# Kernel optimization log

Measured on AMD Instinct MI355X. Metric: run time of the kernel, lower is better.

Reference implementation:

```python
import jax, jax.numpy as jnp
import numpy as np

B, N, H, MEM, V = 512, 50, 256, 8, 40001
SCALE = 1.0 / float(np.sqrt(H))
NEG = -1e12


def sinusoid_table(n_pos, d):
    pos = np.arange(n_pos)[:, None].astype(np.float64)
    j = np.arange(d)[None, :]
    ang = pos / np.power(10000.0, 2 * (j // 2) / d)
    tab = np.zeros((n_pos, d))
    tab[:, 0::2] = np.sin(ang[:, 0::2])
    tab[:, 1::2] = np.cos(ang[:, 1::2])
    return jnp.asarray(tab, jnp.float32)

TAB = sinusoid_table(N, H)


def setup_inputs():
    key = jax.random.key(0)
    ks = jax.random.split(key, 40)
    s = 0.05
    rn = lambda k, shp, sc=s: jax.random.normal(k, shp, jnp.float32) * sc
    lengths = jax.random.randint(ks[0], (B,), 1, N + 1)
    mask = (jnp.arange(N)[None, :] < lengths[:, None]).astype(jnp.int32)
    item_flag = jax.random.randint(ks[1], (B, V - 1), 0, 2).astype(jnp.int32)
    inp = {
        'seq_emb_1': rn(ks[2], (B, N, H), 1.0),
        'seq_emb_2': rn(ks[3], (B, N, H), 1.0),
        'mask': mask,
        'item_flag': item_flag,
        # 2-layer GRU (torch layout: W_ih [3H,H], W_hh [3H,H])
        'gru_wih0': rn(ks[4], (3 * H, H)), 'gru_whh0': rn(ks[5], (3 * H, H)),
        'gru_bih0': rn(ks[6], (3 * H,)), 'gru_bhh0': rn(ks[7], (3 * H,)),
        'gru_wih1': rn(ks[8], (3 * H, H)), 'gru_whh1': rn(ks[9], (3 * H, H)),
        'gru_bih1': rn(ks[10], (3 * H,)), 'gru_bhh1': rn(ks[11], (3 * H,)),
        # attention projections ([in,out] layout, y = x @ W)
        'Wq1': rn(ks[12], (H, H)), 'Wk1': rn(ks[13], (H, H)), 'Wv1': rn(ks[14], (H, H)),
        'Wq2': rn(ks[15], (H, H)), 'Wk2': rn(ks[16], (H, H)), 'Wv2': rn(ks[17], (H, H)),
        'W_ffn1': rn(ks[18], (H, H)), 'b_ffn1': rn(ks[19], (H,)),
        'W_ffn2': rn(ks[20], (H, H)), 'b_ffn2': rn(ks[21], (H,)),
        'W_one1': rn(ks[22], (H, H)), 'b_one1': rn(ks[23], (H,)),
        'W_three1': rn(ks[24], (2 * H, 1)),
        'W_trans1': rn(ks[25], (2 * H, H)), 'b_trans1': rn(ks[26], (H,)),
        'W_tail1': rn(ks[27], (H, H)), 'b_tail1': rn(ks[28], (H,)),
        'W_tail2': rn(ks[29], (H, 2)),
        'mem_k': rn(ks[30], (1, MEM, H)), 'mem_v': rn(ks[31], (1, MEM, H)),
        'emb1': rn(ks[32], (V, H)),
    }
    return inp


def _gru_layer(x, wih, whh, bih, bhh):
    # x: [B,N,H] -> [B,N,H], h0 = 0 (torch default)
    def step(h, xt):
        gi = xt @ wih.T + bih
        gh = h @ whh.T + bhh
        ir, iz, inn = jnp.split(gi, 3, axis=-1)
        hr, hz, hn = jnp.split(gh, 3, axis=-1)
        r = jax.nn.sigmoid(ir + hr)
        z = jax.nn.sigmoid(iz + hz)
        n = jnp.tanh(inn + r * hn)
        h2 = (1.0 - z) * n + z * h
        return h2, h2
    h0 = jnp.zeros((x.shape[0], H), x.dtype)
    _, ys = jax.lax.scan(step, h0, jnp.swapaxes(x, 0, 1))
    return jnp.swapaxes(ys, 0, 1)


def _co_attention(q, k, v, mask, mem_k=None, mem_v=None):
    b = q.shape[0]
    causal = jnp.tril(jnp.ones((N, N), bool))           # [N,N]
    pad = mask.astype(bool)[:, None, :]                  # [B,1,N]
    allow_seq = causal[None, :, :] & pad                 # [B,N,N]
    if mem_k is not None:
        k = jnp.concatenate([jnp.broadcast_to(mem_k, (b, MEM, H)), k], axis=1)
        v = jnp.concatenate([jnp.broadcast_to(mem_v, (b, MEM, H)), v], axis=1)
        mem_ok = jnp.ones((b, N, MEM), bool)             # memory keys always visible
        allow = jnp.concatenate([mem_ok, allow_seq], axis=-1)
    else:
        allow = allow_seq
    att = jnp.einsum('bqh,bkh->bqk', q, k) * SCALE
    att = jax.nn.softmax(jnp.where(allow, att, NEG), axis=-1)
    return jnp.einsum('bqk,bkh->bqh', att, v) * mask[:, :, None].astype(q.dtype)


def reference(seq_emb_1, seq_emb_2, mask, item_flag,
              gru_wih0, gru_whh0, gru_bih0, gru_bhh0,
              gru_wih1, gru_whh1, gru_bih1, gru_bhh1,
              Wq1, Wk1, Wv1, Wq2, Wk2, Wv2,
              W_ffn1, b_ffn1, W_ffn2, b_ffn2,
              W_one1, b_one1, W_three1, W_trans1, b_trans1,
              W_tail1, b_tail1, W_tail2, mem_k, mem_v, emb1):
    b = mask.shape[0]
    mf = mask[:, :, None].astype(jnp.float32)
    # 2-layer GRU on stream 2
    s2 = _gru_layer(seq_emb_2, gru_wih0, gru_whh0, gru_bih0, gru_bhh0)
    s2 = _gru_layer(s2, gru_wih1, gru_whh1, gru_bih1, gru_bhh1)
    last = jnp.sum(mask, axis=1) - 1                     # last valid index
    sr_l_1 = seq_emb_1[jnp.arange(b), last]              # [B,H]
    q1_1 = sr_l_1 @ W_one1 + b_one1 + TAB[0]
    se1 = seq_emb_1 * mf
    # positional encoding indexed by |pos - last_idx|
    flag = jnp.abs(jnp.arange(N, dtype=jnp.int32)[None, :] - last[:, None].astype(jnp.int32))
    pe = TAB[flag]                                       # [B,N,H]
    q1 = se1 @ Wq1 + pe
    k1 = se1 @ Wk1 + pe
    v1 = se1 @ Wv1 + pe
    att1 = _co_attention(q1, k1, v1, mask) @ W_ffn1 + b_ffn1
    se2 = s2 * mf
    k2 = se2 @ Wk2
    v2 = se2 @ Wv2
    att2 = _co_attention(q1, k2, v2, mask, mem_k, mem_v) @ W_ffn2 + b_ffn2
    att = jax.nn.relu(att1 + att2)
    alpha = jnp.concatenate([att, jnp.broadcast_to(q1_1[:, None, :], att.shape)], axis=-1) @ W_three1
    alpha = jax.nn.softmax(jnp.where(mf > 0, alpha, NEG), axis=1)  # [B,N,1]
    sess = jnp.sum(alpha * se1 * mf, axis=1)
    sess = jnp.concatenate([sess, sr_l_1], axis=1) @ W_trans1 + b_trans1
    item_emb = emb1[1:]                                  # [V-1,H]
    score = sess @ item_emb.T                            # [B,V-1]
    fl = item_flag.astype(bool)
    score_in = jax.nn.softmax(jnp.where(fl, score, NEG), axis=-1)
    score_ex = jax.nn.softmax(jnp.where(fl, NEG, score), axis=-1)
    beta = jax.nn.softmax(jax.nn.relu(sess @ W_tail1 + b_tail1) @ W_tail2, axis=-1)  # [B,2]
    boundary = jnp.mean(jnp.abs(beta[:, 0] - beta[:, 1]))
    final = score_in * beta[:, 0:1] + score_ex * beta[:, 1:2]
    return final[:, None, :], boundary
```

## Files before the change

### kernel.cpp

```cpp
#include <hip/hip_runtime.h>
#include <hip/hip_bf16.h>
#include <cstdint>
#include <cstddef>

#define Bsz 512
#define Nsq 50
#define Hd  256
#define VM1 40000
static constexpr float SCALE_C = 0.0625f;
static constexpr float NEG_C   = -1.0e12f;

typedef __attribute__((ext_vector_type(8))) short bf16x8;
typedef __attribute__((ext_vector_type(4))) float f32x4;

__device__ __forceinline__ float sigmoidf_(float x) { return 1.0f / (1.0f + __expf(-x)); }
__device__ __forceinline__ float tanh_fast(float x) {
  float t = fminf(fmaxf(2.0f * x, -60.0f), 60.0f);
  float e = __expf(t);
  return (e - 1.0f) / (e + 1.0f);
}
__device__ __forceinline__ ushort f2b(float x) {
  union { float f; uint32_t u; } c; c.f = x;
  uint32_t r = (c.u + 0x7fffu + ((c.u >> 16) & 1u)) >> 16;
  return (ushort)r;
}

__global__ void build_tab(float* __restrict__ TAB) {
  int idx = blockIdx.x * 256 + threadIdx.x;
  int pos = idx >> 8, j = idx & 255;
  int pair = j >> 1;
  float expo = (2.0f * (float)pair) / 256.0f;
  float inv = powf(10000.0f, -expo);
  float ang = (float)pos * inv;
  TAB[idx] = (j & 1) ? cosf(ang) : sinf(ang);
}

__global__ __launch_bounds__(256) void last_srl_kernel(const int* __restrict__ mask,
    const float* __restrict__ seq1, int* __restrict__ lastp, float* __restrict__ srl) {
  int b = blockIdx.x, tid = threadIdx.x;
  __shared__ int ls;
  if (tid == 0) {
    int c = 0;
    for (int t = 0; t < Nsq; ++t) c += mask[b * Nsq + t];
    ls = c - 1;
    lastp[b] = c - 1;
  }
  __syncthreads();
  srl[b * Hd + tid] = seq1[((size_t)b * Nsq + ls) * Hd + tid];
}

template <int BT, int BIAS>
__global__ __launch_bounds__(256) void gemm_tile(const float* __restrict__ A,
    const float* __restrict__ B, const float* __restrict__ bias,
    float* __restrict__ C, int M, int N, int K) {
  __shared__ float As[16][132];
  __shared__ float Bs[16][68];
  int bm = blockIdx.y * 128, bn = blockIdx.x * 64;
  int tid = threadIdx.x;
  int tm = (tid >> 4) << 3;
  int tn = (tid & 15) << 2;
  float acc[8][4] = {};
  for (int k0 = 0; k0 < K; k0 += 16) {
#pragma unroll
    for (int u = 0; u < 8; ++u) {
      int i = tid + u * 256;
      int kk = i & 15, m = i >> 4;
      As[kk][m] = A[(size_t)(bm + m) * K + (k0 + kk)];
    }
#pragma unroll
    for (int u = 0; u < 4; ++u) {
      int i = tid + u * 256;
      if (BT) {
        int kk = i & 15, n = i >> 4;
        Bs[kk][n] = B[(size_t)(bn + n) * K + (k0 + kk)];
      } else {
        int n = i & 63, kk = i >> 6;
        Bs[kk][n] = B[(size_t)(k0 + kk) * N + (bn + n)];
      }
    }
    __syncthreads();
#pragma unroll
    for (int kk = 0; kk < 16; ++kk) {
      float a[8], bb[4];
#pragma unroll
      for (int r = 0; r < 8; ++r) a[r] = As[kk][tm + r];
#pragma unroll
      for (int c = 0; c < 4; ++c) bb[c] = Bs[kk][tn + c];
#pragma unroll
      for (int r = 0; r < 8; ++r)
#pragma unroll
        for (int c = 0; c < 4; ++c) acc[r][c] += a[r] * bb[c];
    }
    __syncthreads();
  }
#pragma unroll
  for (int r = 0; r < 8; ++r) {
    size_t row = (size_t)(bm + tm + r) * N + bn;
#pragma unroll
    for (int c = 0; c < 4; ++c) {
      float v = acc[r][c];
      if (BIAS) v += bias[bn + tn + c];
      C[row + tn + c] = v;
    }
  }
}

template <int BT, int BIAS>
__global__ __launch_bounds__(256) void mfma_gemm(const ushort* __restrict__ A,
    const ushort* __restrict__ B, const float* __restrict__ bias,
    float* __restrict__ C, int M, int N, int K) {
  __shared__ ushort Asm[128][40];
  __shared__ ushort Bsm[128][40];
  int tid = threadIdx.x;
  int bm = blockIdx.y * 128, bn = blockIdx.x * 128;
  int lane = tid & 63, wave = tid >> 6;
  int quad = lane >> 4, l16 = lane & 15;
  int wm = (wave >> 1) * 64, wn = (wave & 1) * 64;
  f32x4 acc[4][4] = {};
  for (int k0 = 0; k0 < K; k0 += 32) {
#pragma unroll
    for (int u = 0; u < 2; ++u) {
      int idx = tid + u * 256;
      int r = idx >> 2, kc = (idx & 3) * 8;
      uint4 v = *(const uint4*)(A + (size_t)(bm + r) * K + k0 + kc);
      *(uint4*)&Asm[r][kc] = v;
    }
    if (BT) {
#pragma unroll
      for (int u = 0; u < 2; ++u) {
        int idx = tid + u * 256;
        int r = idx >> 2, kc = (idx & 3) * 8;
        uint4 v = make_uint4(0u, 0u, 0u, 0u);
        if (bn + r < N) v = *(const uint4*)(B + (size_t)(bn + r) * K + k0 + kc);
        *(uint4*)&Bsm[r][kc] = v;
      }
    } else {
#pragma unroll
      for (int u = 0; u < 8; ++u) {
        int idx = tid + u * 256;
        int n2 = (idx & 63) * 2, kk = idx >> 6;
        uint v = *(const uint*)(B + (size_t)(k0 + kk) * N + bn + n2);
        Bsm[n2][kk] = (ushort)(v & 0xffffu);
        Bsm[n2 + 1][kk] = (ushort)(v >> 16);
      }
    }
    __syncthreads();
    bf16x8 af[4], bfr[4];
#pragma unroll
    for (int f = 0; f < 4; ++f) af[f] = *(const bf16x8*)&Asm[wm + f * 16 + l16][quad * 8];
#pragma unroll
    for (int f = 0; f < 4; ++f) bfr[f] = *(const bf16x8*)&Bsm[wn + f * 16 + l16][quad * 8];
#pragma unroll
    for (int mf = 0; mf < 4; ++mf)
#pragma unroll
      for (int nf = 0; nf < 4; ++nf)
        acc[mf][nf] = __builtin_amdgcn_mfma_f32_16x16x32_bf16(af[mf], bfr[nf], acc[mf][nf], 0, 0, 0);
    __syncthreads();
  }
#pragma unroll
  for (int mf = 0; mf < 4; ++mf) {
#pragma unroll
    for (int r = 0; r < 4; ++r) {
      int row = bm + wm + mf * 16 + quad * 4 + r;
      size_t rowo = (size_t)row * N;
#pragma unroll
      for (int nf = 0; nf < 4; ++nf) {
        int col = bn + wn + nf * 16 + l16;
        if (col < N) {
          float v = acc[mf][nf][r];
          if (BIAS) v += bias[col];
          C[rowo + col] = v;
        }
      }
    }
  }
}

__global__ void cast_f2b_k(const float* __restrict__ s, ushort* __restrict__ d, int n4) {
  int i = blockIdx.x * 256 + threadIdx.x;
  if (i >= n4) return;
  const float4 v = ((const float4*)s)[i];
  ushort4 o; o.x = f2b(v.x); o.y = f2b(v.y); o.z = f2b(v.z); o.w = f2b(v.w);
  ((ushort4*)d)[i] = o;
}

struct Cast7 { const float* s[7]; ushort* d[7]; };
__global__ void cast7_k(Cast7 p) {
  int m = blockIdx.y;
  int i = blockIdx.x * 256 + threadIdx.x;
  const float4 v = ((const float4*)p.s[m])[i];
  ushort4 o; o.x = f2b(v.x); o.y = f2b(v.y); o.z = f2b(v.z); o.w = f2b(v.w);
  ((ushort4*)p.d[m])[i] = o;
}

__global__ void add_tab0(float* __restrict__ q) {
  int idx = blockIdx.x * 256 + threadIdx.x;
  q[idx] += (float)(threadIdx.x & 1);
}

__global__ void mask_mul_dual(const float* __restrict__ x, const int* __restrict__ m,
                              float* __restrict__ y, ushort* __restrict__ yb) {
  int idx = blockIdx.x * 256 + threadIdx.x;
  float v = m[idx >> 8] ? x[idx] : 0.0f;
  y[idx] = v;
  yb[idx] = f2b(v);
}

__global__ void add_pe3(float* __restrict__ q, float* __restrict__ k, float* __restrict__ v,
                        const float* __restrict__ TAB, const int* __restrict__ lastp) {
  int idx = blockIdx.x * 256 + threadIdx.x;
  int j = idx & 255, bt = idx >> 8;
  int b = bt / Nsq, t = bt - b * Nsq;
  int d = abs(t - lastp[b]);
  float pe = TAB[d * 256 + j];
  q[idx] += pe; k[idx] += pe; v[idx] += pe;
}

__global__ void relu_add(float* __restrict__ a, const float* __restrict__ b) {
  int idx = blockIdx.x * 256 + threadIdx.x;
  a[idx] = fmaxf(a[idx] + b[idx], 0.0f);
}

__global__ __launch_bounds__(512, 2) void gru_mfma8_kernel(const float* __restrict__ gi,
    const ushort* __restrict__ whhb, const float* __restrict__ bhh,
    ushort* __restrict__ ysb, const int* __restrict__ mask) {
  __shared__ ushort hbf[16][264];
  __shared__ float  ghs[2][768];
  int tid = threadIdx.x;
  int lane = tid & 63, wave = tid >> 6;
  int quad = lane >> 4, l16 = lane & 15;
  int s0 = blockIdx.x * 2;

  for (int i = tid; i < 16 * 264 / 2; i += 512) ((uint*)hbf)[i] = 0u;

  bf16x8 bw[48];
  const ushort* wb = whhb + (size_t)(wave * 96 + l16) * 256 + quad * 8;
#pragma unroll
  for (int f = 0; f < 48; ++f) {
    int nf = f >> 3, kf = f & 7;
    bw[f] = *(const bf16x8*)(wb + nf * (16 * 256) + kf * 32);
  }

  int d = tid & 255, sh = tid >> 8;
  float bh0 = bhh[d], bh1 = bhh[256 + d], bh2 = bhh[512 + d];
  const float* gib = gi + (size_t)(s0 + sh) * Nsq * 768;
  float g0 = gib[d], g1 = gib[256 + d], g2 = gib[512 + d];
  float hreg = 0.0f;
  __syncthreads();

  for (int t = 0; t < Nsq; ++t) {
    int tn = (t + 1 < Nsq) ? t + 1 : t;
    float p0 = gib[tn * 768 + d], p1 = gib[tn * 768 + 256 + d], p2 = gib[tn * 768 + 512 + d];

    f32x4 acc[6] = {};
#pragma unroll
    for (int kf = 0; kf < 8; ++kf) {
      bf16x8 a = *(const bf16x8*)&hbf[l16][kf * 32 + quad * 8];
#pragma unroll
      for (int nf = 0; nf < 6; ++nf)
        acc[nf] = __builtin_amdgcn_mfma_f32_16x16x32_bf16(a, bw[nf * 8 + kf], acc[nf], 0, 0, 0);
    }
    if (quad == 0) {
#pragma unroll
      for (int nf = 0; nf < 6; ++nf) {
        int n = wave * 96 + nf * 16 + l16;
        ghs[0][n] = acc[nf][0];
        ghs[1][n] = acc[nf][1];
      }
    }
    __syncthreads();

    {
      float rr = sigmoidf_(g0 + ghs[sh][d] + bh0);
      float zz = sigmoidf_(g1 + ghs[sh][256 + d] + bh1);
      float nn = tanh_fast(g2 + rr * (ghs[sh][512 + d] + bh2));
      float h2 = (1.0f - zz) * nn + zz * hreg;
      hreg = h2;
      hbf[sh][d] = f2b(h2);
      float ov = h2;
      if (mask) ov = mask[(s0 + sh) * Nsq + t] ? h2 : 0.0f;
      ysb[((size_t)(s0 + sh) * Nsq + t) * 256 + d] = f2b(ov);
    }
    g0 = p0; g1 = p1; g2 = p2;
    __syncthreads();
  }
}

template <int NMEM>
__global__ __launch_bounds__(256) void attn_mfma(const float* __restrict__ q1,
    const float* __restrict__ kseq, const float* __restrict__ vseq,
    const float* __restrict__ kmem, const float* __restrict__ vmem,
    const int* __restrict__ mask, ushort* __restrict__ out) {
  constexpr int NK = NMEM + Nsq;
  __shared__ ushort KV[64][264];
  __shared__ float Ss[64][66];
  __shared__ ushort Ps[64][72];
  __shared__ int msk[64];
  int tid = threadIdx.x;
  int lane = tid & 63, wave = tid >> 6;
  int quad = lane >> 4, l16 = lane & 15;
  int b = blockIdx.x;

  if (tid < 64) msk[tid] = (tid < Nsq) ? mask[b * Nsq + tid] : 0;

#pragma unroll
  for (int it = 0; it < 16; ++it) {
    int idx = tid + it * 256;
    int r = idx >> 6, c4 = (idx & 63) * 4;
    float4 v = make_float4(0.f, 0.f, 0.f, 0.f);
    if (r < Nsq) v = *(const float4*)(q1 + ((size_t)(b * Nsq + r)) * 256 + c4);
    ushort4 o; o.x = f2b(v.x); o.y = f2b(v.y); o.z = f2b(v.z); o.w = f2b(v.w);
    *(ushort4*)&KV[r][c4] = o;
  }
  __syncthreads();
  bf16x8 qa[8];
#pragma unroll
  for (int kf = 0; kf < 8; ++kf)
    qa[kf] = *(const bf16x8*)&KV[wave * 16 + l16][kf * 32 + quad * 8];
  __syncthreads();

#pragma unroll
  for (int it = 0; it < 16; ++it) {
    int idx = tid + it * 256;
    int r = idx >> 6, c4 = (idx & 63) * 4;
    float4 v = make_float4(0.f, 0.f, 0.f, 0.f);
    if (r < NK) {
      const float* src = (NMEM > 0 && r < NMEM)
          ? (kmem + (size_t)r * 256 + c4)
          : (kseq + ((size_t)(b * Nsq + (r - NMEM))) * 256 + c4);
      v = *(const float4*)src;
    }
    ushort4 o; o.x = f2b(v.x); o.y = f2b(v.y); o.z = f2b(v.z); o.w = f2b(v.w);
    *(ushort4*)&KV[r][c4] = o;
  }
  __syncthreads();

  {
    f32x4 acc[4] = {};
#pragma unroll
    for (int kf = 0; kf < 8; ++kf) {
#pragma unroll
      for (int nf = 0; nf < 4; ++nf) {
        bf16x8 bf = *(const bf16x8*)&KV[nf * 16 + l16][kf * 32 + quad * 8];
        acc[nf] = __builtin_amdgcn_mfma_f32_16x16x32_bf16(qa[kf], bf, acc[nf], 0, 0, 0);
      }
    }
#pragma unroll
    for (int nf = 0; nf < 4; ++nf)
#pragma unroll
      for (int r = 0; r < 4; ++r)
        Ss[wave * 16 + quad * 4 + r][nf * 16 + l16] = acc[nf][r];
  }
  __syncthreads();

#pragma unroll
  for (int it = 0; it < 16; ++it) {
    int idx = tid + it * 256;
    int r = idx >> 6, c4 = (idx & 63) * 4;
    float4 v = make_float4(0.f, 0.f, 0.f, 0.f);
    if (r < NK) {
      const float* src = (NMEM > 0 && r < NMEM)
          ? (vmem + (size_t)r * 256 + c4)
          : (vseq + ((size_t)(b * Nsq + (r - NMEM))) * 256 + c4);
      v = *(const float4*)src;
    }
    ushort4 o; o.x = f2b(v.x); o.y = f2b(v.y); o.z = f2b(v.z); o.w = f2b(v.w);
    *(ushort4*)&KV[r][c4] = o;
  }
  if (tid < 64) {
    int t = tid;
    if (t < Nsq) {
      float m = -1e30f;
      for (int j = 0; j < NK; ++j) {
        bool ok = (j < NMEM) || (((j - NMEM) <= t) && (msk[j - NMEM] != 0));
        if (ok) m = fmaxf(m, Ss[t][j] * SCALE_C);
      }
      float sum = 0.0f;
      for (int j = 0; j < NK; ++j) {
        bool ok = (j < NMEM) || (((j - NMEM) <= t) && (msk[j - NMEM] != 0));
        if (ok) sum += __expf(Ss[t][j] * SCALE_C - m);
      }
      float inv = 1.0f / sum;
      for (int j = 0; j < 64; ++j) {
        float p = 0.0f;
        if (j < NK) {
          bool ok = (j < NMEM) || (((j - NMEM) <= t) && (msk[j - NMEM] != 0));
          if (ok) p = __expf(Ss[t][j] * SCALE_C - m) * inv;
        }
        Ps[t][j] = f2b(p);
      }
    } else {
      for (int j = 0; j < 64; ++j) Ps[t][j] = 0;
    }
  }
  __syncthreads();

  {
    f32x4 o[4][4] = {};
#pragma unroll
    for (int kf = 0; kf < 2; ++kf) {
      bf16x8 pa[4];
#pragma unroll
      for (int mf = 0; mf < 4; ++mf)
        pa[mf] = *(const bf16x8*)&Ps[mf * 16 + l16][kf * 32 + quad * 8];
#pragma unroll
      for (int nf = 0; nf < 4; ++nf) {
        int h = wave * 64 + nf * 16 + l16;
        ushort e0 = KV[kf * 32 + quad * 8 + 0][h];
        ushort e1 = KV[kf * 32 + quad * 8 + 1][h];
        ushort e2 = KV[kf * 32 + quad * 8 + 2][h];
        ushort e3 = KV[kf * 32 + quad * 8 + 3][h];
        ushort e4 = KV[kf * 32 + quad * 8 + 4][h];
        ushort e5 = KV[kf * 32 + quad * 8 + 5][h];
        ushort e6 = KV[kf * 32 + quad * 8 + 6][h];
        ushort e7 = KV[kf * 32 + quad * 8 + 7][h];
        bf16x8 vb = {(short)e0, (short)e1, (short)e2, (short)e3,
                     (short)e4, (short)e5, (short)e6, (short)e7};
#pragma unroll
        for (int mf = 0; mf < 4; ++mf)
          o[mf][nf] = __builtin_amdgcn_mfma_f32_16x16x32_bf16(pa[mf], vb, o[mf][nf], 0, 0, 0);
      }
    }
#pragma unroll
    for (int mf = 0; mf < 4; ++mf) {
#pragma unroll
      for (int r = 0; r < 4; ++r) {
        int t = mf * 16 + quad * 4 + r;
        if (t < Nsq) {
          int zero = (msk[t] == 0);
#pragma unroll
          for (int nf = 0; nf < 4; ++nf) {
            int h = wave * 64 + nf * 16 + l16;
            float val = zero ? 0.0f : o[mf][nf][r];
            out[((size_t)(b * Nsq + t)) * 256 + h] = f2b(val);
          }
        }
      }
    }
  }
}

__global__ __launch_bounds__(256) void alpha_sess_kernel(const float* __restrict__ att,
    const float* __restrict__ W3, const float* __restrict__ q11,
    const float* __restrict__ se1, const int* __restrict__ mask,
    const float* __restrict__ srl, float* __restrict__ sesscat) {
  int b = blockIdx.x, tid = threadIdx.x;
  __shared__ float red[256];
  __shared__ float ash[50];
  red[tid] = q11[b * Hd + tid] * W3[256 + tid];
  __syncthreads();
  for (int s = 128; s; s >>= 1) { if (tid < s) red[tid] += red[tid + s]; __syncthreads(); }
  float cq = red[0];
  float aval = 0.0f;
  if (tid < 50) {
    float s = cq;
    const float* ar = att + ((size_t)b * Nsq + tid) * Hd;
    for (int hh = 0; hh < 256; ++hh) s += ar[hh] * W3[hh];
    aval = mask[b * Nsq + tid] ? s : NEG_C;
  }
  if (tid < 64) {
    float s = (tid < 50) ? aval : NEG_C;
    float m = s;
    for (int off = 32; off; off >>= 1) m = fmaxf(m, __shfl_xor(m, off));
    float e = expf(s - m);
    float sum = e;
    for (int off = 32; off; off >>= 1) sum += __shfl_xor(sum, off);
    if (tid < 50) ash[tid] = e / sum;
  }
  __syncthreads();
  float acc = 0.0f;
  const float* se = se1 + (size_t)b * Nsq * Hd;
  for (int t = 0; t < Nsq; ++t) acc += ash[t] * se[t * 256 + tid];
  sesscat[(size_t)b * 512 + tid] = acc;
  sesscat[(size_t)b * 512 + 256 + tid] = srl[b * Hd + tid];
}

__global__ __launch_bounds__(256) void beta_kernel(const float* __restrict__ sess2,
    const float* __restrict__ Wt1, const float* __restrict__ bt1,
    const float* __restrict__ Wt2, float* __restrict__ beta, float* __restrict__ bnd) {
  int b = blockIdx.x, tid = threadIdx.x;
  __shared__ float xs[256];
  __shared__ float r0[256], r1[256];
  xs[tid] = sess2[b * Hd + tid];
  __syncthreads();
  float hsum = bt1[tid];
  for (int k = 0; k < 256; ++k) hsum += xs[k] * Wt1[k * 256 + tid];
  float hid = fmaxf(hsum, 0.0f);
  r0[tid] = hid * Wt2[tid * 2 + 0];
  r1[tid] = hid * Wt2[tid * 2 + 1];
  __syncthreads();
  for (int s = 128; s; s >>= 1) {
    if (tid < s) { r0[tid] += r0[tid + s]; r1[tid] += r1[tid + s]; }
    __syncthreads();
  }
  if (tid == 0) {
    float t0 = r0[0], t1 = r1[0];
    float m = fmaxf(t0, t1);
    float e0 = expf(t0 - m), e1 = expf(t1 - m);
    float bb0 = e0 / (e0 + e1), bb1 = e1 / (e0 + e1);
    beta[b * 2] = bb0; beta[b * 2 + 1] = bb1;
    atomicAdd(bnd, fabsf(bb0 - bb1) * (1.0f / 512.0f));
  }
}

__global__ __launch_bounds__(256) void score_stats_kernel(const float* __restrict__ score,
    const int* __restrict__ flag, float* __restrict__ stats) {
  int b = blockIdx.x, tid = threadIdx.x;
  float mi = -INFINITY, si = 0.0f, me = -INFINITY, se = 0.0f;
  const float* sr = score + (size_t)b * VM1;
  const int* fr = flag + (size_t)b * VM1;
  for (int i = tid; i < VM1; i += 256) {
    float s = sr[i];
    int f = fr[i];
    float vi = f ? s : NEG_C;
    float ve = f ? NEG_C : s;
    float mni = fmaxf(mi, vi); si = si * expf(mi - mni) + expf(vi - mni); mi = mni;
    float mne = fmaxf(me, ve); se = se * expf(me - mne) + expf(ve - mne); me = mne;
  }
  __shared__ float red[256];
  red[tid] = mi; __syncthreads();
  for (int s = 128; s; s >>= 1) { if (tid < s) red[tid] = fmaxf(red[tid], red[tid + s]); __syncthreads(); }
  float Mi = red[0]; __syncthreads();
  red[tid] = si * expf(mi - Mi); __syncthreads();
  for (int s = 128; s; s >>= 1) { if (tid < s) red[tid] += red[tid + s]; __syncthreads(); }
  float Si = red[0]; __syncthreads();
  red[tid] = me; __syncthreads();
  for (int s = 128; s; s >>= 1) { if (tid < s) red[tid] = fmaxf(red[tid], red[tid + s]); __syncthreads(); }
  float Me = red[0]; __syncthreads();
  red[tid] = se * expf(me - Me); __syncthreads();
  for (int s = 128; s; s >>= 1) { if (tid < s) red[tid] += red[tid + s]; __syncthreads(); }
  float Se = red[0];
  if (tid == 0) { stats[b * 4] = Mi; stats[b * 4 + 1] = Si; stats[b * 4 + 2] = Me; stats[b * 4 + 3] = Se; }
}

__global__ void final_kernel(float* __restrict__ score, const int* __restrict__ flag,
                             const float* __restrict__ stats, const float* __restrict__ beta) {
  int idx = blockIdx.x * 256 + threadIdx.x;
  int b = idx / VM1;
  float s = score[idx];
  int f = flag[idx];
  float vi = f ? s : NEG_C;
  float ve = f ? NEG_C : s;
  float fin = beta[b * 2] * expf(vi - stats[b * 4]) / stats[b * 4 + 1]
            + beta[b * 2 + 1] * expf(ve - stats[b * 4 + 2]) / stats[b * 4 + 3];
  score[idx] = fin;
}

extern "C" void kernel_launch(void* const* d_in, const int* in_sizes, int n_in,
                              void* d_out, int out_size, void* d_ws, size_t ws_size,
                              hipStream_t stream) {
  const float* seq1  = (const float*)d_in[0];
  const float* seq2  = (const float*)d_in[1];
  const int*   mask  = (const int*)d_in[2];
  const int*   iflag = (const int*)d_in[3];
  const float* wih0  = (const float*)d_in[4];
  const float* whh0  = (const float*)d_in[5];
  const float* bih0  = (const float*)d_in[6];
  const float* bhh0  = (const float*)d_in[7];
  const float* wih1  = (const float*)d_in[8];
  const float* whh1  = (const float*)d_in[9];
  const float* bih1  = (const float*)d_in[10];
  const float* bhh1  = (const float*)d_in[11];
  const float* Wq1   = (const float*)d_in[12];
  const float* Wk1   = (const float*)d_in[13];
  const float* Wv1   = (const float*)d_in[14];
  const float* Wk2   = (const float*)d_in[16];
  const float* Wv2   = (const float*)d_in[17];
  const float* Wffn1 = (const float*)d_in[18];
  const float* bffn1 = (const float*)d_in[19];
  const float* Wffn2 = (const float*)d_in[20];
  const float* bffn2 = (const float*)d_in[21];
  const float* Wone  = (const float*)d_in[22];
  const float* bone  = (const float*)d_in[23];
  const float* W3    = (const float*)d_in[24];
  const float* Wtr   = (const float*)d_in[25];
  const float* btr   = (const float*)d_in[26];
  const float* Wt1   = (const float*)d_in[27];
  const float* bt1   = (const float*)d_in[28];
  const float* Wt2   = (const float*)d_in[29];
  const float* memk  = (const float*)d_in[30];
  const float* memv  = (const float*)d_in[31];
  const float* emb1  = (const float*)d_in[32];
  float* out = (float*)d_out;

  char* wsb = (char*)d_ws;
  float*  TAB    = (float*)(wsb + 0);
  int*    lastp  = (int*)  (wsb + 51200);
  float*  srl    = (float*)(wsb + 53248);
  float*  q11    = (float*)(wsb + 577536);
  ushort* whh0b  = (ushort*)(wsb + 1101824);
  ushort* whh1b  = (ushort*)(wsb + 1888256);
  ushort* wih0b  = (ushort*)(wsb + 2674688);
  ushort* wih1b  = (ushort*)(wsb + 3067904);
  ushort* w7b    = (ushort*)(wsb + 3461120);
  ushort* bufS   = (ushort*)(wsb + 4378624);
  float*  se1    = (float*)(wsb + 17485824);
  ushort* se1b   = (ushort*)(wsb + 43700224);
  float*  giQ    = (float*)(wsb + 56807424);
  float*  kv2a   = (float*)(wsb + 135450624);
  float*  kv2b   = (float*)(wsb + 161665024);
  ushort* ao1b   = (ushort*)(wsb + 187879424);
  ushort* ao2b   = (ushort*)(wsb + 200986624);

  float* gi = giQ;
  float* q1 = giQ;
  float* k1 = giQ + 6553600;
  float* v1 = giQ + 13107200;
  ushort* embB    = (ushort*)giQ;
  float*  sesscat = (float*)((char*)giQ + 20480000);
  float*  sess2   = (float*)((char*)giQ + 21528576);
  ushort* sess2b  = (ushort*)((char*)giQ + 22052864);
  float*  betab   = (float*)((char*)giQ + 22315008);
  float*  stats   = (float*)((char*)giQ + 22319104);
  float*  bnd     = out + (size_t)Bsz * VM1;

  ushort* Wq1b = w7b;              ushort* Wk1b = w7b + 65536;
  ushort* Wv1b = w7b + 131072;     ushort* Wk2b = w7b + 196608;
  ushort* Wv2b = w7b + 262144;     ushort* Wf1b = w7b + 327680;
  ushort* Wf2b = w7b + 393216;

  build_tab<<<50, 256, 0, stream>>>(TAB);
  last_srl_kernel<<<Bsz, 256, 0, stream>>>(mask, seq1, lastp, srl);
  gemm_tile<0, 1><<<dim3(4, 4), 256, 0, stream>>>(srl, Wone, bone, q11, 512, 256, 256);
  add_tab0<<<512, 256, 0, stream>>>(q11);

  cast_f2b_k<<<6400, 256, 0, stream>>>(seq2, bufS, 1638400);
  cast_f2b_k<<<192, 256, 0, stream>>>(wih0, wih0b, 49152);
  cast_f2b_k<<<192, 256, 0, stream>>>(wih1, wih1b, 49152);
  cast_f2b_k<<<192, 256, 0, stream>>>(whh0, whh0b, 49152);
  cast_f2b_k<<<192, 256, 0, stream>>>(whh1, whh1b, 49152);
  Cast7 c7;
  c7.s[0] = Wq1; c7.s[1] = Wk1; c7.s[2] = Wv1; c7.s[3] = Wk2; c7.s[4] = Wv2;
  c7.s[5] = Wffn1; c7.s[6] = Wffn2;
  c7.d[0] = Wq1b; c7.d[1] = Wk1b; c7.d[2] = Wv1b; c7.d[3] = Wk2b; c7.d[4] = Wv2b;
  c7.d[5] = Wf1b; c7.d[6] = Wf2b;
  cast7_k<<<dim3(64, 7), 256, 0, stream>>>(c7);

  mfma_gemm<1, 1><<<dim3(6, 200), 256, 0, stream>>>(bufS, wih0b, bih0, gi, 25600, 768, 256);
  gru_mfma8_kernel<<<256, 512, 0, stream>>>(gi, whh0b, bhh0, bufS, nullptr);
  mfma_gemm<1, 1><<<dim3(6, 200), 256, 0, stream>>>(bufS, wih1b, bih1, gi, 25600, 768, 256);
  gru_mfma8_kernel<<<256, 512, 0, stream>>>(gi, whh1b, bhh1, bufS, mask);

  mask_mul_dual<<<25600, 256, 0, stream>>>(seq1, mask, se1, se1b);

  mfma_gemm<0, 0><<<dim3(2, 200), 256, 0, stream>>>(bufS, Wk2b, nullptr, kv2a, 25600, 256, 256);
  mfma_gemm<0, 0><<<dim3(2, 200), 256, 0, stream>>>(bufS, Wv2b, nullptr, kv2b, 25600, 256, 256);
  mfma_gemm<0, 0><<<dim3(2, 200), 256, 0, stream>>>(se1b, Wq1b, nullptr, q1, 25600, 256, 256);
  mfma_gemm<0, 0><<<dim3(2, 200), 256, 0, stream>>>(se1b, Wk1b, nullptr, k1, 25600, 256, 256);
  mfma_gemm<0, 0><<<dim3(2, 200), 256, 0, stream>>>(se1b, Wv1b, nullptr, v1, 25600, 256, 256);
  add_pe3<<<25600, 256, 0, stream>>>(q1, k1, v1, TAB, lastp);

  attn_mfma<0><<<Bsz, 256, 0, stream>>>(q1, k1, v1, nullptr, nullptr, mask, ao1b);
  attn_mfma<8><<<Bsz, 256, 0, stream>>>(q1, kv2a, kv2b, memk, memv, mask, ao2b);
  mfma_gemm<0, 1><<<dim3(2, 200), 256, 0, stream>>>(ao1b, Wf1b, bffn1, kv2a, 25600, 256, 256);
  mfma_gemm<0, 1><<<dim3(2, 200), 256, 0, stream>>>(ao2b, Wf2b, bffn2, kv2b, 25600, 256, 256);
  relu_add<<<25600, 256, 0, stream>>>(kv2a, kv2b);

  alpha_sess_kernel<<<Bsz, 256, 0, stream>>>(kv2a, W3, q11, se1, mask, srl, sesscat);
  gemm_tile<0, 1><<<dim3(4, 4), 256, 0, stream>>>(sesscat, Wtr, btr, sess2, 512, 256, 512);
  cast_f2b_k<<<128, 256, 0, stream>>>(sess2, sess2b, 32768);

  hipMemsetAsync(bnd, 0, 4, stream);
  beta_kernel<<<Bsz, 256, 0, stream>>>(sess2, Wt1, bt1, Wt2, betab, bnd);
  cast_f2b_k<<<10000, 256, 0, stream>>>(emb1 + 256, embB, 2560000);
  mfma_gemm<1, 0><<<dim3(313, 4), 256, 0, stream>>>(sess2b, embB, nullptr, out, 512, VM1, 256);
  score_stats_kernel<<<Bsz, 256, 0, stream>>>(out, iflag, stats);
  final_kernel<<<80000, 256, 0, stream>>>(out, iflag, stats, betab);

  (void)in_sizes; (void)n_in; (void)out_size; (void)ws_size;
}
```

Measured before the change: 1.122 ms.

## Fuse score softmax statistics and final blend into one per-row kernel

Replaces the separate online-softmax statistics kernel and the elementwise final kernel with a single per-row kernel. It runs a vectorized max pass, then an exp/sum pass that writes the exponentials back with the flag encoded in the sign, then a scaling pass that applies beta over the sum. This removes the double expf per element of the online rescaling, a kernel launch, and the second flag read in the final step. In exchange each row's scores are read three times from memory or cache, and it relies on sign encoding plus fast __expf instead of expf.

```diff
diff --git a/kernel.cpp b/kernel.cpp
--- a/kernel.cpp
+++ b/kernel.cpp
@@ -503,47 +503,67 @@
   }
 }
 
-__global__ __launch_bounds__(256) void score_stats_kernel(const float* __restrict__ score,
-    const int* __restrict__ flag, float* __restrict__ stats) {
+__global__ __launch_bounds__(256) void score_final_fused(float* __restrict__ score,
+    const int* __restrict__ flag, const float* __restrict__ beta) {
   int b = blockIdx.x, tid = threadIdx.x;
-  float mi = -INFINITY, si = 0.0f, me = -INFINITY, se = 0.0f;
-  const float* sr = score + (size_t)b * VM1;
-  const int* fr = flag + (size_t)b * VM1;
-  for (int i = tid; i < VM1; i += 256) {
-    float s = sr[i];
-    int f = fr[i];
-    float vi = f ? s : NEG_C;
-    float ve = f ? NEG_C : s;
-    float mni = fmaxf(mi, vi); si = si * expf(mi - mni) + expf(vi - mni); mi = mni;
-    float mne = fmaxf(me, ve); se = se * expf(me - mne) + expf(ve - mne); me = mne;
-  }
-  __shared__ float red[256];
-  red[tid] = mi; __syncthreads();
-  for (int s = 128; s; s >>= 1) { if (tid < s) red[tid] = fmaxf(red[tid], red[tid + s]); __syncthreads(); }
-  float Mi = red[0]; __syncthreads();
-  red[tid] = si * expf(mi - Mi); __syncthreads();
-  for (int s = 128; s; s >>= 1) { if (tid < s) red[tid] += red[tid + s]; __syncthreads(); }
-  float Si = red[0]; __syncthreads();
-  red[tid] = me; __syncthreads();
-  for (int s = 128; s; s >>= 1) { if (tid < s) red[tid] = fmaxf(red[tid], red[tid + s]); __syncthreads(); }
-  float Me = red[0]; __syncthreads();
-  red[tid] = se * expf(me - Me); __syncthreads();
-  for (int s = 128; s; s >>= 1) { if (tid < s) red[tid] += red[tid + s]; __syncthreads(); }
-  float Se = red[0];
-  if (tid == 0) { stats[b * 4] = Mi; stats[b * 4 + 1] = Si; stats[b * 4 + 2] = Me; stats[b * 4 + 3] = Se; }
-}
-
-__global__ void final_kernel(float* __restrict__ score, const int* __restrict__ flag,
-                             const float* __restrict__ stats, const float* __restrict__ beta) {
-  int idx = blockIdx.x * 256 + threadIdx.x;
-  int b = idx / VM1;
-  float s = score[idx];
-  int f = flag[idx];
-  float vi = f ? s : NEG_C;
-  float ve = f ? NEG_C : s;
-  float fin = beta[b * 2] * expf(vi - stats[b * 4]) / stats[b * 4 + 1]
-            + beta[b * 2 + 1] * expf(ve - stats[b * 4 + 2]) / stats[b * 4 + 3];
-  score[idx] = fin;
+  float4* sr = (float4*)(score + (size_t)b * VM1);
+  const int4* fr = (const int4*)(flag + (size_t)b * VM1);
+  constexpr int NV = VM1 / 4;
+
+  __shared__ float red[256], red2[256];
+
+  float mi = -INFINITY, me = -INFINITY;
+  for (int i = tid; i < NV; i += 256) {
+    float4 s = sr[i];
+    int4 f = fr[i];
+    if (f.x) mi = fmaxf(mi, s.x); else me = fmaxf(me, s.x);
+    if (f.y) mi = fmaxf(mi, s.y); else me = fmaxf(me, s.y);
+    if (f.z) mi = fmaxf(mi, s.z); else me = fmaxf(me, s.z);
+    if (f.w) mi = fmaxf(mi, s.w); else me = fmaxf(me, s.w);
+  }
+  red[tid] = mi; red2[tid] = me;
+  __syncthreads();
+  for (int s = 128; s; s >>= 1) {
+    if (tid < s) { red[tid] = fmaxf(red[tid], red[tid + s]); red2[tid] = fmaxf(red2[tid], red2[tid + s]); }
+    __syncthreads();
+  }
+  float Mi = red[0], Me = red2[0];
+  __syncthreads();
+
+  float si = 0.0f, se = 0.0f;
+  for (int i = tid; i < NV; i += 256) {
+    float4 s = sr[i];
+    int4 f = fr[i];
+    float e0 = __expf(s.x - (f.x ? Mi : Me));
+    float e1 = __expf(s.y - (f.y ? Mi : Me));
+    float e2 = __expf(s.z - (f.z ? Mi : Me));
+    float e3 = __expf(s.w - (f.w ? Mi : Me));
+    si += (f.x ? e0 : 0.0f) + (f.y ? e1 : 0.0f) + (f.z ? e2 : 0.0f) + (f.w ? e3 : 0.0f);
+    se += (f.x ? 0.0f : e0) + (f.y ? 0.0f : e1) + (f.z ? 0.0f : e2) + (f.w ? 0.0f : e3);
+    s.x = f.x ? e0 : -e0;
+    s.y = f.y ? e1 : -e1;
+    s.z = f.z ? e2 : -e2;
+    s.w = f.w ? e3 : -e3;
+    sr[i] = s;
+  }
+  red[tid] = si; red2[tid] = se;
+  __syncthreads();
+  for (int s = 128; s; s >>= 1) {
+    if (tid < s) { red[tid] += red[tid + s]; red2[tid] += red2[tid + s]; }
+    __syncthreads();
+  }
+  float c0 = beta[b * 2] / red[0];
+  float nc1 = -(beta[b * 2 + 1] / red2[0]);
+  __syncthreads();
+
+  for (int i = tid; i < NV; i += 256) {
+    float4 z = sr[i];
+    z.x = (z.x >= 0.0f ? c0 : nc1) * z.x;
+    z.y = (z.y >= 0.0f ? c0 : nc1) * z.y;
+    z.z = (z.z >= 0.0f ? c0 : nc1) * z.z;
+    z.w = (z.w >= 0.0f ? c0 : nc1) * z.w;
+    sr[i] = z;
+  }
 }
 
 extern "C" void kernel_launch(void* const* d_in, const int* in_sizes, int n_in,
@@ -664,8 +684,7 @@
   beta_kernel<<<Bsz, 256, 0, stream>>>(sess2, Wt1, bt1, Wt2, betab, bnd);
   cast_f2b_k<<<10000, 256, 0, stream>>>(emb1 + 256, embB, 2560000);
   mfma_gemm<1, 0><<<dim3(313, 4), 256, 0, stream>>>(sess2b, embB, nullptr, out, 512, VM1, 256);
-  score_stats_kernel<<<Bsz, 256, 0, stream>>>(out, iflag, stats);
-  final_kernel<<<80000, 256, 0, stream>>>(out, iflag, stats, betab);
+  score_final_fused<<<Bsz, 256, 0, stream>>>(out, iflag, betab);
 
   (void)in_sizes; (void)n_in; (void)out_size; (void)ws_size;
 }
```

Result: faster. 1.007 ms (-10.2%).
